# Optimization experiments

Measured on AMD Instinct MI355X. Metric: run time of the kernel, lower is better.

## Reference

```python
import jax, jax.numpy as jnp
import numpy as np

B, NPG, K, H = 64, 2048, 10, 64   # graphs, points-per-graph, kNN, hidden
N = B * NPG
EPS = 1e-5  # PairNorm eps


def _lin_init(key, fan_in, fan_out):
    kw, kb = jax.random.split(key)
    s = 1.0 / np.sqrt(fan_in)
    W = jax.random.uniform(kw, (fan_in, fan_out), jnp.float32, -s, s)
    b = jax.random.uniform(kb, (fan_out,), jnp.float32, -s, s)
    return W, b


def setup_inputs() -> dict:
    key = jax.random.key(0)
    ks = jax.random.split(key, 6)
    pos = jax.random.normal(ks[0], (N, 2), jnp.float32)
    batch = jnp.repeat(jnp.arange(B, dtype=jnp.int32), NPG)
    W1, b1 = _lin_init(ks[1], 2, H)
    W2, b2 = _lin_init(ks[2], H + 2, H)
    W3, b3 = _lin_init(ks[3], H + 2, H)
    Wl1, bl1 = _lin_init(ks[4], H, H)
    Wl2, bl2 = _lin_init(ks[5], H, 2)
    return dict(pos=pos, batch=batch, W1=W1, b1=b1, W2=W2, b2=b2,
                W3=W3, b3=b3, Wl1=Wl1, bl1=bl1, Wl2=Wl2, bl2=bl2)


def pair_norm(x):
    # PyG PairNorm, mode='PN', scale=1: center, then divide by rms of row norms
    xc = x - x.mean(axis=0, keepdims=True)
    return xc / jnp.sqrt(EPS + (xc ** 2).sum(axis=-1).mean())


def knn_edges(pos):
    # equal-sized graphs laid out contiguously -> batched pairwise distances
    p = pos.reshape(B, NPG, 2)
    d2 = ((p[:, :, None, :] - p[:, None, :, :]) ** 2).sum(-1)   # [B, n, n]
    d2 = jnp.where(jnp.eye(NPG, dtype=bool), jnp.inf, d2)       # loop=False
    _, idx = jax.lax.top_k(-d2, K)                              # [B, n, K]
    offs = (jnp.arange(NPG * B, step=NPG) if False else (jnp.arange(B) * NPG))[:, None, None]
    src = (idx + offs).reshape(-1)                              # neighbor j
    dst = jnp.broadcast_to(jnp.arange(N).reshape(B, NPG, 1), (B, NPG, K)).reshape(-1)
    # PointNetConv(add_self_loops=True): append self edges once, reuse in all convs
    sl = jnp.arange(N)
    return jnp.concatenate([src, sl]), jnp.concatenate([dst, sl])


def pointnet_conv(x, pos, src, dst, W, b):
    rel = pos[src] - pos[dst]                                    # [E, 2]
    msg = rel if x is None else jnp.concatenate([x[src], rel], axis=-1)
    msg = msg @ W + b                                            # local_nn
    return jax.ops.segment_max(msg, dst, num_segments=N)         # aggr='max'


def reference(pos, batch, W1, b1, W2, b2, W3, b3, Wl1, bl1, Wl2, bl2):
    src, dst = knn_edges(pos)
    h1 = pair_norm(jax.nn.relu(pointnet_conv(None, pos, src, dst, W1, b1)))
    h2 = pair_norm(jax.nn.relu(pointnet_conv(h1, pos, src, dst, W2, b2)))
    h3 = pair_norm(jax.nn.relu(pointnet_conv(h2, pos, src, dst, W3, b3)))
    g = h3.reshape(B, NPG, H).max(axis=1)                        # global_max_pool
    g = jax.nn.relu(g @ Wl1 + bl1)
    # dropout p=0.2 is identity in eval mode
    return g @ Wl2 + bl2                                         # [B, 2]
```

## Files before the change

kernel.cpp:

```cpp
#include <hip/hip_runtime.h>
#include <math.h>

#define NTOT   131072
#define NPG    2048
#define NB     64
#define KNNK   10
#define HID    64
#define EPSPN  1e-5f

__device__ inline float rdlane(float v, int l) {
    return __int_as_float(__builtin_amdgcn_readlane(__float_as_int(v), l));
}

__global__ __launch_bounds__(1024) void sort_kernel(const float2* __restrict__ pos,
        float2* __restrict__ spos, unsigned short* __restrict__ y2xg)
{
    __shared__ float2   sp[NPG];
    __shared__ unsigned sk[NPG];
    __shared__ unsigned sv[NPG];
    const int base = blockIdx.x * NPG;
    const int tid  = threadIdx.x;

    for (int t = tid; t < NPG; t += 1024) {
        unsigned u = __float_as_uint(pos[base + t].x);
        sk[t] = (u & 0x80000000u) ? ~u : (u | 0x80000000u);
        sv[t] = (unsigned)t;
    }
    __syncthreads();
    for (int k = 2; k <= NPG; k <<= 1) {
        for (int j = k >> 1; j > 0; j >>= 1) {
            int i = ((tid & ~(j - 1)) << 1) | (tid & (j - 1));
            int l = i + j;
            bool up = ((i & k) == 0);
            unsigned a = sk[i], b = sk[l];
            if ((a > b) == up) {
                sk[i] = b; sk[l] = a;
                unsigned t2 = sv[i]; sv[i] = sv[l]; sv[l] = t2;
            }
            __syncthreads();
        }
    }
    for (int t = tid; t < NPG; t += 1024) sp[t] = pos[base + sv[t]];
    __syncthreads();
    for (int t = tid; t < NPG; t += 1024) spos[base + t] = sp[t];

    for (int t = tid; t < NPG; t += 1024) {
        unsigned u = __float_as_uint(sp[t].y);
        sk[t] = (u & 0x80000000u) ? ~u : (u | 0x80000000u);
        sv[t] = (unsigned)t;
    }
    __syncthreads();
    for (int k = 2; k <= NPG; k <<= 1) {
        for (int j = k >> 1; j > 0; j >>= 1) {
            int i = ((tid & ~(j - 1)) << 1) | (tid & (j - 1));
            int l = i + j;
            bool up = ((i & k) == 0);
            unsigned a = sk[i], b = sk[l];
            if ((a > b) == up) {
                sk[i] = b; sk[l] = a;
                unsigned t2 = sv[i]; sv[i] = sv[l]; sv[l] = t2;
            }
            __syncthreads();
        }
    }
    for (int t = tid; t < NPG; t += 1024) y2xg[base + t] = (unsigned short)sv[t];
}

#define INSERT(INS, D2, JJ) do {                                              \
    const bool ins_ = (INS);                                                  \
    bd[9] = ins_ ? (D2) : bd[9];                                              \
    bi[9] = ins_ ? (JJ) : bi[9];                                              \
    _Pragma("unroll")                                                         \
    for (int kk = 0; kk < 9; ++kk) {                                          \
        bool sw_ = bd[kk] > bd[9];                                            \
        float tv_ = bd[kk]; int ti_ = bi[kk];                                 \
        bd[kk] = sw_ ? bd[9] : bd[kk]; bi[kk] = sw_ ? bi[9] : bi[kk];         \
        bd[9]  = sw_ ? tv_  : bd[9];   bi[9]  = sw_ ? ti_  : bi[9];           \
    }                                                                         \
} while (0)

#define CSWAP(A, B) do {                                                      \
    bool sw_ = bd[A] > bd[B];                                                 \
    float tf_ = bd[A]; int ti_ = bi[A];                                       \
    bd[A] = sw_ ? bd[B] : bd[A]; bi[A] = sw_ ? bi[B] : bi[A];                 \
    bd[B] = sw_ ? tf_  : bd[B]; bi[B] = sw_ ? ti_  : bi[B];                   \
} while (0)

__global__ __launch_bounds__(256) void knn_kernel(const float2* __restrict__ spos,
        const unsigned short* __restrict__ y2xg, unsigned short* __restrict__ knn)
{
    __shared__ float2 sarr[NPG];
    __shared__ unsigned short y2x[NPG];
    __shared__ unsigned short x2y[NPG];
    const int tid  = threadIdx.x;
    const int g    = blockIdx.x >> 4;
    const int base = g * NPG;

    for (int t = tid; t < NPG; t += 256) {
        sarr[t] = spos[base + t];
        y2x[t]  = y2xg[base + t];
    }
    __syncthreads();
    for (int t = tid; t < NPG; t += 256) {
        x2y[(int)y2x[t]] = (unsigned short)t;
    }
    __syncthreads();

    const int ql = ((blockIdx.x & 15) << 7) + (tid >> 1);
    const int d  = tid & 1;
    const float qx = sarr[ql].x, qy = sarr[ql].y;
    const int py = (int)x2y[ql];

    float span_x = sarr[min(ql + 8, NPG - 1)].x - sarr[max(ql - 8, 0)].x;
    float span_y = sarr[(int)y2x[min(py + 8, NPG - 1)]].y
                 - sarr[(int)y2x[max(py - 8, 0)]].y;
    const bool cy   = span_y > span_x;
    const int  r    = cy ? py : ql;
    const int  limit = d ? (NPG - 1 - r) : r;
    const int  sign  = d ? 1 : -1;

    float bd[KNNK];
    int   bi[KNNK];
#pragma unroll
    for (int k = 0; k < KNNK; ++k) { bd[k] = INFINITY; bi[k] = 0; }

    int s = 1;
    bool alive = (limit >= 1);
    while (__any(alive)) {
        int j0 = min(NPG - 1, max(0, r + sign * s));
        int j1 = min(NPG - 1, max(0, r + sign * (s + 1)));
        int j2 = min(NPG - 1, max(0, r + sign * (s + 2)));
        int j3 = min(NPG - 1, max(0, r + sign * (s + 3)));
        int x0 = cy ? (int)y2x[j0] : j0;
        int x1 = cy ? (int)y2x[j1] : j1;
        int x2 = cy ? (int)y2x[j2] : j2;
        int x3 = cy ? (int)y2x[j3] : j3;
        float2 p0 = sarr[x0];
        float2 p1 = sarr[x1];
        float2 p2 = sarr[x2];
        float2 p3 = sarr[x3];
        float dx0 = __fsub_rn(qx, p0.x), dy0 = __fsub_rn(qy, p0.y);
        float dx1 = __fsub_rn(qx, p1.x), dy1 = __fsub_rn(qy, p1.y);
        float dx2 = __fsub_rn(qx, p2.x), dy2 = __fsub_rn(qy, p2.y);
        float dx3 = __fsub_rn(qx, p3.x), dy3 = __fsub_rn(qy, p3.y);
        float xs0 = __fmul_rn(dx0, dx0), ys0 = __fmul_rn(dy0, dy0);
        float xs1 = __fmul_rn(dx1, dx1), ys1 = __fmul_rn(dy1, dy1);
        float xs2 = __fmul_rn(dx2, dx2), ys2 = __fmul_rn(dy2, dy2);
        float xs3 = __fmul_rn(dx3, dx3), ys3 = __fmul_rn(dy3, dy3);
        float d20 = __fadd_rn(xs0, ys0);
        float d21 = __fadd_rn(xs1, ys1);
        float d22 = __fadd_rn(xs2, ys2);
        float d23 = __fadd_rn(xs3, ys3);
        bool v0 = alive && (s     <= limit);
        bool v1 = alive && (s + 1 <= limit);
        bool v2 = alive && (s + 2 <= limit);
        bool v3 = alive && (s + 3 <= limit);
        bool pre = (v0 && d20 < bd[9]) || (v1 && d21 < bd[9]) ||
                   (v2 && d22 < bd[9]) || (v3 && d23 < bd[9]);
        if (__any(pre)) {
            INSERT(v0 && (d20 < bd[9]), d20, x0);
            INSERT(v1 && (d21 < bd[9]), d21, x1);
            INSERT(v2 && (d22 < bd[9]), d22, x2);
            INSERT(v3 && (d23 < bd[9]), d23, x3);
        }
        float thr = fminf(bd[9], __shfl_xor(bd[9], 1));
        float pr3 = cy ? ys3 : xs3;
        alive = alive && (s + 4 <= limit) && (pr3 < thr);
        s += 4;
    }

#pragma unroll
    for (int ph = 0; ph < 10; ++ph) {
        if ((ph & 1) == 0) { CSWAP(0,1); CSWAP(2,3); CSWAP(4,5); CSWAP(6,7); CSWAP(8,9); }
        else               { CSWAP(1,2); CSWAP(3,4); CSWAP(5,6); CSWAP(7,8); }
    }
    float obd[KNNK]; int obi[KNNK];
#pragma unroll
    for (int k = 0; k < KNNK; ++k) {
        obd[k] = __shfl_xor(bd[k], 1);
        obi[k] = __shfl_xor(bi[k], 1);
    }
    if (d == 0) {
        const int row = (base + ql) * KNNK;
#pragma unroll
        for (int k = 0; k < KNNK; ++k) {
            bool ta = bd[k] < obd[9 - k];
            int idx = ta ? bi[k] : obi[9 - k];
            knn[row + k] = (unsigned short)idx;
        }
    }
}

#define GEMM64(V, OUTEXPR) do {                                               \
    float a0 = 0.f, a1 = 0.f, a2 = 0.f, a3 = 0.f;                             \
    _Pragma("unroll")                                                         \
    for (int k = 0; k < 16; ++k) {                                            \
        a0 = fmaf(rdlane((V), k),      wcol[k],      a0);                     \
        a1 = fmaf(rdlane((V), k + 16), wcol[k + 16], a1);                     \
        a2 = fmaf(rdlane((V), k + 32), wcol[k + 32], a2);                     \
        a3 = fmaf(rdlane((V), k + 48), wcol[k + 48], a3);                     \
    }                                                                         \
    (OUTEXPR) = (a0 + a1) + (a2 + a3);                                        \
} while (0)

#define WSWZ() (((blockIdx.x & 7) << 7) | (blockIdx.x >> 3))

__global__ __launch_bounds__(256) void conv1_kernel(const float2* __restrict__ spos,
        const unsigned short* __restrict__ knn, const float* __restrict__ W1,
        const float* __restrict__ b1, const float* __restrict__ W2a,
        float* __restrict__ out, float* __restrict__ st)
{
    __shared__ float red[256];
    __shared__ float2 sarr[NPG];
    const int tid  = threadIdx.x;
    const int lane = tid & 63, w = tid >> 6;
    const int wg   = WSWZ();
    const int i0   = wg * 128 + w * 32;
    const int base = (wg >> 4) << 11;
    const int il0  = i0 - base;
    const float w0 = W1[lane], w1 = W1[HID + lane], bb = b1[lane];
    float wcol[HID];
#pragma unroll
    for (int k = 0; k < HID; ++k) wcol[k] = W2a[k * HID + lane];
    for (int t = tid; t < NPG; t += 256) sarr[t] = spos[base + t];
    __syncthreads();
    float cs = 0.f, ss = 0.f;
    for (int r = 0; r < 32; ++r) {
        const int il = il0 + r;
        float2 pi = sarr[il];
        float acc = bb;
#pragma unroll
        for (int e = 0; e < KNNK; ++e) {
            int j = (int)knn[(size_t)(base + il) * KNNK + e];
            float2 pj = sarr[j];
            acc = fmaxf(acc, fmaf(pj.x - pi.x, w0, fmaf(pj.y - pi.y, w1, bb)));
        }
        float v = fmaxf(acc, 0.f);
        cs += v; ss = fmaf(v, v, ss);
        GEMM64(v, out[(size_t)(base + il) * HID + lane]);
    }
    red[tid] = cs; __syncthreads();
    if (tid < 64) atomicAdd(&st[tid], red[tid] + red[tid + 64] + red[tid + 128] + red[tid + 192]);
#pragma unroll
    for (int o = 32; o > 0; o >>= 1) ss += __shfl_xor(ss, o, 64);
    __syncthreads();
    if (lane == 0) red[w] = ss;
    __syncthreads();
    if (tid == 0) atomicAdd(&st[64], red[0] + red[1] + red[2] + red[3]);
}

__global__ __launch_bounds__(64) void stats_kernel(float* __restrict__ st,
        const float* __restrict__ Wn, const float* __restrict__ bn)
{
    const int c = threadIdx.x;
    float mean = st[c] * (1.0f / (float)NTOT);
    st[128 + c] = mean;
    float m2 = mean * mean;
#pragma unroll
    for (int o = 32; o > 0; o >>= 1) m2 += __shfl_xor(m2, o, 64);
    float s = (st[64] - (float)NTOT * m2) * (1.0f / (float)NTOT);
    s = fmaxf(s, 0.f);
    float inv = 1.0f / sqrtf(EPSPN + s);
    if (c == 0) st[66] = inv;
    if (Wn != nullptr) {
        float dot = 0.f;
#pragma unroll
        for (int k = 0; k < HID; ++k) dot = fmaf(rdlane(mean, k), Wn[k * HID + c], dot);
        st[192 + c] = bn[c] - inv * dot;
    }
}

__global__ __launch_bounds__(256, 2) void convG2_kernel(const float2* __restrict__ spos,
        const unsigned short* __restrict__ knn, const float* __restrict__ hw,
        const float* __restrict__ Wb, const float* __restrict__ Wna,
        const float* __restrict__ stin, float* __restrict__ out,
        float* __restrict__ stout)
{
    __shared__ float red[256];
    __shared__ float2 sarr[NPG];
    const int tid  = threadIdx.x;
    const int lane = tid & 63, w = tid >> 6;
    const int wg   = WSWZ();
    const int i0   = wg * 128 + w * 32;
    const int base = (wg >> 4) << 11;
    const float wb0 = Wb[lane], wb1 = Wb[HID + lane];
    const float inv = stin[66], offs = stin[192 + lane];
    float wcol[HID];
#pragma unroll
    for (int k = 0; k < HID; ++k) wcol[k] = Wna[k * HID + lane];
    for (int t = tid; t < NPG; t += 256) sarr[t] = spos[base + t];
    __syncthreads();

    const unsigned* kb = (const unsigned*)knn;
    unsigned idx0[5], idx1[5];
    float hwC[KNNK], hwN[KNNK], hwS, hwSN;
#pragma unroll
    for (int e = 0; e < 5; ++e) idx0[e] = kb[(size_t)i0 * 5 + e];
#pragma unroll
    for (int e = 0; e < 5; ++e) idx1[e] = kb[(size_t)(i0 + 1) * 5 + e];
#pragma unroll
    for (int e = 0; e < 5; ++e) {
        int ja = base + (int)(idx0[e] & 0xFFFFu);
        int jb = base + (int)(idx0[e] >> 16);
        hwC[2 * e]     = hw[(size_t)ja * HID + lane];
        hwC[2 * e + 1] = hw[(size_t)jb * HID + lane];
    }
    hwS = hw[(size_t)i0 * HID + lane];

    float cs = 0.f, ss = 0.f;
    for (int r = 0; r < 32; ++r) {
        const int i = i0 + r;
        const int il = i - base;
        unsigned idx2[5];
        if (r + 2 < 32) {
#pragma unroll
            for (int e = 0; e < 5; ++e) idx2[e] = kb[(size_t)(i + 2) * 5 + e];
        }
        float2 pi = sarr[il];
        float acc = fmaf(inv, hwS, offs);
#pragma unroll
        for (int e = 0; e < 5; ++e) {
            int la = (int)(idx0[e] & 0xFFFFu);
            int lb = (int)(idx0[e] >> 16);
            float2 pa = sarr[la];
            float2 pb = sarr[lb];
            float xwa = fmaf(inv, hwC[2 * e],     offs);
            float xwb = fmaf(inv, hwC[2 * e + 1], offs);
            acc = fmaxf(acc, fmaf(pa.x - pi.x, wb0, fmaf(pa.y - pi.y, wb1, xwa)));
            acc = fmaxf(acc, fmaf(pb.x - pi.x, wb0, fmaf(pb.y - pi.y, wb1, xwb)));
        }
        if (r + 1 < 32) {
#pragma unroll
            for (int e = 0; e < 5; ++e) {
                int ja = base + (int)(idx1[e] & 0xFFFFu);
                int jb = base + (int)(idx1[e] >> 16);
                hwN[2 * e]     = hw[(size_t)ja * HID + lane];
                hwN[2 * e + 1] = hw[(size_t)jb * HID + lane];
            }
            hwSN = hw[(size_t)(i + 1) * HID + lane];
        }
        float v = fmaxf(acc, 0.f);
        cs += v; ss = fmaf(v, v, ss);
        GEMM64(v, out[(size_t)i * HID + lane]);
#pragma unroll
        for (int e = 0; e < 5; ++e) idx0[e] = idx1[e];
        if (r + 2 < 32) {
#pragma unroll
            for (int e = 0; e < 5; ++e) idx1[e] = idx2[e];
        }
#pragma unroll
        for (int e = 0; e < KNNK; ++e) hwC[e] = hwN[e];
        hwS = hwSN;
    }
    red[tid] = cs; __syncthreads();
    if (tid < 64) atomicAdd(&stout[tid], red[tid] + red[tid + 64] + red[tid + 128] + red[tid + 192]);
#pragma unroll
    for (int o = 32; o > 0; o >>= 1) ss += __shfl_xor(ss, o, 64);
    __syncthreads();
    if (lane == 0) red[w] = ss;
    __syncthreads();
    if (tid == 0) atomicAdd(&stout[64], red[0] + red[1] + red[2] + red[3]);
}

__global__ __launch_bounds__(256, 2) void convB3_kernel(const float2* __restrict__ spos,
        const unsigned short* __restrict__ knn, const float* __restrict__ hw,
        const float* __restrict__ Wb, const float* __restrict__ stin,
        float* __restrict__ stout, float* __restrict__ gmax)
{
    __shared__ float red[256];
    __shared__ float2 sarr[NPG];
    const int tid  = threadIdx.x;
    const int lane = tid & 63, w = tid >> 6;
    const int wg   = WSWZ();
    const int i0   = wg * 128 + w * 32;
    const int base = (wg >> 4) << 11;
    const float wb0 = Wb[lane], wb1 = Wb[HID + lane];
    const float inv = stin[66], offs = stin[192 + lane];
    for (int t = tid; t < NPG; t += 256) sarr[t] = spos[base + t];
    __syncthreads();

    const unsigned* kb = (const unsigned*)knn;
    unsigned idx0[5], idx1[5];
    float hwC[KNNK], hwN[KNNK], hwS, hwSN;
#pragma unroll
    for (int e = 0; e < 5; ++e) idx0[e] = kb[(size_t)i0 * 5 + e];
#pragma unroll
    for (int e = 0; e < 5; ++e) idx1[e] = kb[(size_t)(i0 + 1) * 5 + e];
#pragma unroll
    for (int e = 0; e < 5; ++e) {
        int ja = base + (int)(idx0[e] & 0xFFFFu);
        int jb = base + (int)(idx0[e] >> 16);
        hwC[2 * e]     = hw[(size_t)ja * HID + lane];
        hwC[2 * e + 1] = hw[(size_t)jb * HID + lane];
    }
    hwS = hw[(size_t)i0 * HID + lane];

    float cs = 0.f, ss = 0.f, gm = 0.f;
    for (int r = 0; r < 32; ++r) {
        const int i = i0 + r;
        const int il = i - base;
        unsigned idx2[5];
        if (r + 2 < 32) {
#pragma unroll
            for (int e = 0; e < 5; ++e) idx2[e] = kb[(size_t)(i + 2) * 5 + e];
        }
        float2 pi = sarr[il];
        float acc = fmaf(inv, hwS, offs);
#pragma unroll
        for (int e = 0; e < 5; ++e) {
            int la = (int)(idx0[e] & 0xFFFFu);
            int lb = (int)(idx0[e] >> 16);
            float2 pa = sarr[la];
            float2 pb = sarr[lb];
            float xwa = fmaf(inv, hwC[2 * e],     offs);
            float xwb = fmaf(inv, hwC[2 * e + 1], offs);
            acc = fmaxf(acc, fmaf(pa.x - pi.x, wb0, fmaf(pa.y - pi.y, wb1, xwa)));
            acc = fmaxf(acc, fmaf(pb.x - pi.x, wb0, fmaf(pb.y - pi.y, wb1, xwb)));
        }
        if (r + 1 < 32) {
#pragma unroll
            for (int e = 0; e < 5; ++e) {
                int ja = base + (int)(idx1[e] & 0xFFFFu);
                int jb = base + (int)(idx1[e] >> 16);
                hwN[2 * e]     = hw[(size_t)ja * HID + lane];
                hwN[2 * e + 1] = hw[(size_t)jb * HID + lane];
            }
            hwSN = hw[(size_t)(i + 1) * HID + lane];
        }
        float v = fmaxf(acc, 0.f);
        cs += v; ss = fmaf(v, v, ss);
        gm = fmaxf(gm, v);
#pragma unroll
        for (int e = 0; e < 5; ++e) idx0[e] = idx1[e];
        if (r + 2 < 32) {
#pragma unroll
            for (int e = 0; e < 5; ++e) idx1[e] = idx2[e];
        }
#pragma unroll
        for (int e = 0; e < KNNK; ++e) hwC[e] = hwN[e];
        hwS = hwSN;
    }
    red[tid] = cs; __syncthreads();
    if (tid < 64) atomicAdd(&stout[tid], red[tid] + red[tid + 64] + red[tid + 128] + red[tid + 192]);
#pragma unroll
    for (int o = 32; o > 0; o >>= 1) ss += __shfl_xor(ss, o, 64);
    __syncthreads();
    if (lane == 0) red[w] = ss;
    __syncthreads();
    if (tid == 0) atomicAdd(&stout[64], red[0] + red[1] + red[2] + red[3]);
    const int g = (wg >> 4);
    atomicMax((int*)gmax + g * HID + lane, __float_as_int(gm));
}

__global__ __launch_bounds__(64) void head_kernel(const float* __restrict__ gmax,
        const float* __restrict__ st3, const float* __restrict__ Wl1,
        const float* __restrict__ bl1, const float* __restrict__ Wl2,
        const float* __restrict__ bl2, float* __restrict__ out)
{
    const int b = blockIdx.x, c = threadIdx.x;
    float gv = (gmax[b * HID + c] - st3[128 + c]) * st3[66];
    float a = bl1[c];
#pragma unroll
    for (int k = 0; k < HID; ++k) a = fmaf(rdlane(gv, k), Wl1[k * HID + c], a);
    float h1 = fmaxf(a, 0.f);
    float o = bl2[c & 1];
#pragma unroll
    for (int k = 0; k < HID; ++k) o = fmaf(rdlane(h1, k), Wl2[k * 2 + (c & 1)], o);
    if (c < 2) out[b * 2 + c] = o;
}

extern "C" void kernel_launch(void* const* d_in, const int* in_sizes, int n_in,
                              void* d_out, int out_size, void* d_ws, size_t ws_size,
                              hipStream_t stream)
{
    const float2* pos = (const float2*)d_in[0];
    const float* W1  = (const float*)d_in[2];
    const float* b1  = (const float*)d_in[3];
    const float* W2  = (const float*)d_in[4];
    const float* b2  = (const float*)d_in[5];
    const float* W3  = (const float*)d_in[6];
    const float* b3  = (const float*)d_in[7];
    const float* Wl1 = (const float*)d_in[8];
    const float* bl1 = (const float*)d_in[9];
    const float* Wl2 = (const float*)d_in[10];
    const float* bl2 = (const float*)d_in[11];
    float* out = (float*)d_out;

    char* p = (char*)d_ws;
    unsigned short* knn  = (unsigned short*)p;  p += (size_t)NTOT * KNNK * 2;
    float2* spos = (float2*)p;                  p += (size_t)NTOT * 8;
    unsigned short* y2xg = (unsigned short*)p;  p += (size_t)NTOT * 2;
    float* bufA  = (float*)p;                   p += (size_t)NTOT * HID * 4;
    float* bufB  = (float*)p;                   p += (size_t)NTOT * HID * 4;
    float* st    = (float*)p;
    float* gmax  = st + 768;

    hipMemsetAsync(st, 0, (768 + NB * HID) * sizeof(float), stream);

    sort_kernel<<<NB, 1024, 0, stream>>>(pos, spos, y2xg);
    knn_kernel <<<NTOT / 128, 256, 0, stream>>>(spos, y2xg, knn);

    conv1_kernel<<<NTOT / 128, 256, 0, stream>>>(spos, knn, W1, b1, W2, bufA, st);
    stats_kernel<<<1, 64, 0, stream>>>(st, W2, b2);

    convG2_kernel<<<NTOT / 128, 256, 0, stream>>>(spos, knn, bufA, W2 + 64 * HID,
                                                  W3, st, bufB, st + 256);
    stats_kernel<<<1, 64, 0, stream>>>(st + 256, W3, b3);

    convB3_kernel<<<NTOT / 128, 256, 0, stream>>>(spos, knn, bufB, W3 + 64 * HID,
                                                  st + 256, st + 512, gmax);
    stats_kernel<<<1, 64, 0, stream>>>(st + 512, nullptr, nullptr);

    head_kernel<<<NB, 64, 0, stream>>>(gmax, st + 512, Wl1, bl1, Wl2, bl2, out);
}
```

Baseline: 306.5 us.

## Replace per-row readlane GEMM with batched bf16x3 MFMA via LDS staging

Each wave now stages its 32 activated rows in shared memory and runs one 32x64x64 product per wave with 32x32x16 bf16 MFMA instructions, instead of 64 readlane-FMA steps per row. The hi/lo bf16 split (three MFMAs per tile) keeps near-fp32 accuracy. This cuts VALU and scalar readlane work in conv1 and convG2. In exchange it adds LDS traffic, split-conversion cost, a larger shared footprint that may reduce occupancy, and a strided output store pattern.

```diff
diff --git a/kernel.cpp b/kernel.cpp
--- a/kernel.cpp
+++ b/kernel.cpp
@@ -10,6 +10,22 @@
 
 __device__ inline float rdlane(float v, int l) {
     return __int_as_float(__builtin_amdgcn_readlane(__float_as_int(v), l));
+}
+
+typedef short v8bf  __attribute__((ext_vector_type(8)));
+typedef float v16f  __attribute__((ext_vector_type(16)));
+
+__device__ inline unsigned short f2bf(float f) {
+    unsigned u = __float_as_uint(f);
+    return (unsigned short)((u + 0x7FFFu + ((u >> 16) & 1u)) >> 16);
+}
+__device__ inline float bf2f(unsigned short s) {
+    return __uint_as_float((unsigned)s << 16);
+}
+__device__ inline void split_bf(float v, short& hi, short& lo) {
+    unsigned short h = f2bf(v);
+    hi = (short)h;
+    lo = (short)f2bf(v - bf2f(h));
 }
 
 __global__ __launch_bounds__(1024) void sort_kernel(const float2* __restrict__ pos,
@@ -191,17 +207,59 @@
     }
 }
 
-#define GEMM64(V, OUTEXPR) do {                                               \
-    float a0 = 0.f, a1 = 0.f, a2 = 0.f, a3 = 0.f;                             \
-    _Pragma("unroll")                                                         \
-    for (int k = 0; k < 16; ++k) {                                            \
-        a0 = fmaf(rdlane((V), k),      wcol[k],      a0);                     \
-        a1 = fmaf(rdlane((V), k + 16), wcol[k + 16], a1);                     \
-        a2 = fmaf(rdlane((V), k + 32), wcol[k + 32], a2);                     \
-        a3 = fmaf(rdlane((V), k + 48), wcol[k + 48], a3);                     \
-    }                                                                         \
-    (OUTEXPR) = (a0 + a1) + (a2 + a3);                                        \
-} while (0)
+__device__ inline void build_bfrags(const float* __restrict__ Wa, int lane,
+                                    v8bf (&bhi)[4][2], v8bf (&blo)[4][2])
+{
+    const int cl = lane & 31, kg = lane >> 5;
+#pragma unroll
+    for (int kt = 0; kt < 4; ++kt)
+#pragma unroll
+        for (int nt = 0; nt < 2; ++nt)
+#pragma unroll
+            for (int j = 0; j < 8; ++j) {
+                float wv = Wa[(kt * 16 + kg * 8 + j) * HID + nt * 32 + cl];
+                short h, l;
+                split_bf(wv, h, l);
+                bhi[kt][nt][j] = h; blo[kt][nt][j] = l;
+            }
+}
+
+__device__ inline void mfma_gemm_store(const float* vrow,
+        const v8bf (&bhi)[4][2], const v8bf (&blo)[4][2],
+        int lane, int i0, float* __restrict__ out)
+{
+    const int cl = lane & 31, kg = lane >> 5;
+    v16f acc0, acc1;
+#pragma unroll
+    for (int q = 0; q < 16; ++q) { acc0[q] = 0.f; acc1[q] = 0.f; }
+#pragma unroll
+    for (int kt = 0; kt < 4; ++kt) {
+        const float4 f0 = *(const float4*)(vrow + cl * 68 + kt * 16 + kg * 8);
+        const float4 f1 = *(const float4*)(vrow + cl * 68 + kt * 16 + kg * 8 + 4);
+        v8bf ah, al;
+        short h, l;
+        split_bf(f0.x, h, l); ah[0] = h; al[0] = l;
+        split_bf(f0.y, h, l); ah[1] = h; al[1] = l;
+        split_bf(f0.z, h, l); ah[2] = h; al[2] = l;
+        split_bf(f0.w, h, l); ah[3] = h; al[3] = l;
+        split_bf(f1.x, h, l); ah[4] = h; al[4] = l;
+        split_bf(f1.y, h, l); ah[5] = h; al[5] = l;
+        split_bf(f1.z, h, l); ah[6] = h; al[6] = l;
+        split_bf(f1.w, h, l); ah[7] = h; al[7] = l;
+        acc0 = __builtin_amdgcn_mfma_f32_32x32x16_bf16(ah, bhi[kt][0], acc0, 0, 0, 0);
+        acc0 = __builtin_amdgcn_mfma_f32_32x32x16_bf16(al, bhi[kt][0], acc0, 0, 0, 0);
+        acc0 = __builtin_amdgcn_mfma_f32_32x32x16_bf16(ah, blo[kt][0], acc0, 0, 0, 0);
+        acc1 = __builtin_amdgcn_mfma_f32_32x32x16_bf16(ah, bhi[kt][1], acc1, 0, 0, 0);
+        acc1 = __builtin_amdgcn_mfma_f32_32x32x16_bf16(al, bhi[kt][1], acc1, 0, 0, 0);
+        acc1 = __builtin_amdgcn_mfma_f32_32x32x16_bf16(ah, blo[kt][1], acc1, 0, 0, 0);
+    }
+#pragma unroll
+    for (int reg = 0; reg < 16; ++reg) {
+        int rowc = (reg & 3) + 8 * (reg >> 2) + 4 * kg;
+        out[(size_t)(i0 + rowc) * HID + cl]      = acc0[reg];
+        out[(size_t)(i0 + rowc) * HID + 32 + cl] = acc1[reg];
+    }
+}
 
 #define WSWZ() (((blockIdx.x & 7) << 7) | (blockIdx.x >> 3))
 
@@ -212,6 +270,7 @@
 {
     __shared__ float red[256];
     __shared__ float2 sarr[NPG];
+    __shared__ __align__(16) float vbuf[4][32 * 68];
     const int tid  = threadIdx.x;
     const int lane = tid & 63, w = tid >> 6;
     const int wg   = WSWZ();
@@ -219,9 +278,8 @@
     const int base = (wg >> 4) << 11;
     const int il0  = i0 - base;
     const float w0 = W1[lane], w1 = W1[HID + lane], bb = b1[lane];
-    float wcol[HID];
-#pragma unroll
-    for (int k = 0; k < HID; ++k) wcol[k] = W2a[k * HID + lane];
+    v8bf bhi[4][2], blo[4][2];
+    build_bfrags(W2a, lane, bhi, blo);
     for (int t = tid; t < NPG; t += 256) sarr[t] = spos[base + t];
     __syncthreads();
     float cs = 0.f, ss = 0.f;
@@ -237,8 +295,10 @@
         }
         float v = fmaxf(acc, 0.f);
         cs += v; ss = fmaf(v, v, ss);
-        GEMM64(v, out[(size_t)(base + il) * HID + lane]);
-    }
+        vbuf[w][r * 68 + lane] = v;
+    }
+    mfma_gemm_store(vbuf[w], bhi, blo, lane, i0, out);
+
     red[tid] = cs; __syncthreads();
     if (tid < 64) atomicAdd(&st[tid], red[tid] + red[tid + 64] + red[tid + 128] + red[tid + 192]);
 #pragma unroll
@@ -278,6 +338,7 @@
 {
     __shared__ float red[256];
     __shared__ float2 sarr[NPG];
+    __shared__ __align__(16) float vbuf[4][32 * 68];
     const int tid  = threadIdx.x;
     const int lane = tid & 63, w = tid >> 6;
     const int wg   = WSWZ();
@@ -285,9 +346,8 @@
     const int base = (wg >> 4) << 11;
     const float wb0 = Wb[lane], wb1 = Wb[HID + lane];
     const float inv = stin[66], offs = stin[192 + lane];
-    float wcol[HID];
-#pragma unroll
-    for (int k = 0; k < HID; ++k) wcol[k] = Wna[k * HID + lane];
+    v8bf bhi[4][2], blo[4][2];
+    build_bfrags(Wna, lane, bhi, blo);
     for (int t = tid; t < NPG; t += 256) sarr[t] = spos[base + t];
     __syncthreads();
 
@@ -341,7 +401,7 @@
         }
         float v = fmaxf(acc, 0.f);
         cs += v; ss = fmaf(v, v, ss);
-        GEMM64(v, out[(size_t)i * HID + lane]);
+        vbuf[w][r * 68 + lane] = v;
 #pragma unroll
         for (int e = 0; e < 5; ++e) idx0[e] = idx1[e];
         if (r + 2 < 32) {
@@ -352,6 +412,8 @@
         for (int e = 0; e < KNNK; ++e) hwC[e] = hwN[e];
         hwS = hwSN;
     }
+    mfma_gemm_store(vbuf[w], bhi, blo, lane, i0, out);
+
     red[tid] = cs; __syncthreads();
     if (tid < 64) atomicAdd(&stout[tid], red[tid] + red[tid + 64] + red[tid + 128] + red[tid + 192]);
 #pragma unroll
```

New measurement: 286.4 us. 1.07x faster.
